# Optimization experiments

Hardware: AMD Instinct MI355X
Metric: run time of the kernel (lower is better)

Reference implementation:

```python
import jax, jax.numpy as jnp
import numpy as np

D_MODEL = 1024
NHEAD = 16
D_FF = 4096
LN_EPS = 1e-5


def _layer_norm(x, g, b):
    mu = jnp.mean(x, axis=-1, keepdims=True)
    var = jnp.mean(jnp.square(x - mu), axis=-1, keepdims=True)
    return (x - mu) * jax.lax.rsqrt(var + LN_EPS) * g + b


def setup_inputs() -> dict:
    key = jax.random.key(0)
    ks = jax.random.split(key, 12)
    d, f = D_MODEL, D_FF
    s = 1.0 / np.sqrt(d)
    inp = {
        "src": jax.random.normal(ks[0], (2, 2048, d), dtype=jnp.float32),
        "Wq": jax.random.uniform(ks[1], (d, d), jnp.float32, -s, s),
        "bq": jnp.zeros((d,), jnp.float32),
        "Wk": jax.random.uniform(ks[2], (d, d), jnp.float32, -s, s),
        "bk": jnp.zeros((d,), jnp.float32),
        "Wv": jax.random.uniform(ks[3], (d, d), jnp.float32, -s, s),
        "bv": jnp.zeros((d,), jnp.float32),
        "Wo": jax.random.uniform(ks[4], (d, d), jnp.float32, -s, s),
        "bo": jnp.zeros((d,), jnp.float32),
        "W1": jax.random.uniform(ks[5], (d, f), jnp.float32, -s, s),
        "b1": jnp.zeros((f,), jnp.float32),
        "W2": jax.random.uniform(ks[6], (f, d), jnp.float32, -1.0 / np.sqrt(f), 1.0 / np.sqrt(f)),
        "b2": jnp.zeros((d,), jnp.float32),
        "ln1_g": jnp.ones((d,), jnp.float32),
        "ln1_b": jnp.zeros((d,), jnp.float32),
        "ln2_g": jnp.ones((d,), jnp.float32),
        "ln2_b": jnp.zeros((d,), jnp.float32),
    }
    return inp


def reference(src, Wq, bq, Wk, bk, Wv, bv, Wo, bo, W1, b1, W2, b2,
              ln1_g, ln1_b, ln2_g, ln2_b):
    B, S, D = src.shape
    H = NHEAD
    hd = D // H
    # QKV projections, split into heads: [B, H, S, hd]
    q = (src @ Wq + bq).reshape(B, S, H, hd).transpose(0, 2, 1, 3)
    k = (src @ Wk + bk).reshape(B, S, H, hd).transpose(0, 2, 1, 3)
    v = (src @ Wv + bv).reshape(B, S, H, hd).transpose(0, 2, 1, 3)
    # Explicit full-score attention (no mask branch), as in source.
    scores = jnp.einsum("bhqd,bhkd->bhqk", q, k) / jnp.sqrt(jnp.asarray(hd, src.dtype))
    attn = jax.nn.softmax(scores, axis=-1)
    ctx = jnp.einsum("bhqk,bhkd->bhqd", attn, v)
    ctx = ctx.transpose(0, 2, 1, 3).reshape(B, S, D)
    src2 = ctx @ Wo + bo
    x = _layer_norm(src + src2, ln1_g, ln1_b)
    ff = jax.nn.relu(x @ W1 + b1) @ W2 + b2
    out = _layer_norm(x + ff, ln2_g, ln2_b)
    return out
```

## Files before the change

### kernel.cpp

```cpp
#include <hip/hip_runtime.h>
#include <cstdint>
#include <cstddef>

#define SEQ 2048
#define BATCH 2
#define ROWS (BATCH * SEQ)

typedef __attribute__((ext_vector_type(8))) short short8;
typedef __attribute__((ext_vector_type(4))) float f32x4;
typedef __attribute__((ext_vector_type(16))) float f32x16;
typedef __attribute__((ext_vector_type(8))) _Float16 half8;
typedef __attribute__((ext_vector_type(2))) __fp16 fp16x2;

__device__ __forceinline__ unsigned short f2bf(float f) {
  union { float f; uint32_t u; } v; v.f = f;
  uint32_t r = v.u + 0x7fffu + ((v.u >> 16) & 1u);
  return (unsigned short)(r >> 16);
}

__device__ __forceinline__ unsigned short bf2h(unsigned short b) {
  union { uint32_t u; float f; } v; v.u = ((uint32_t)b) << 16;
  union { _Float16 h; unsigned short u; } o; o.h = (_Float16)v.f;
  return o.u;
}

__device__ __forceinline__ void async16(const void* g, void* l) {
  __builtin_amdgcn_global_load_lds((const __attribute__((address_space(1))) void*)g,
                                   (__attribute__((address_space(3))) void*)l, 16, 0, 0);
}

__global__ __launch_bounds__(256) void f2bf_kernel(const float* __restrict__ in,
                                                   unsigned short* __restrict__ out) {
  size_t i = ((size_t)blockIdx.x * 256 + threadIdx.x) * 4;
  float4 vv = *(const float4*)(in + i);
  ushort4 o;
  o.x = f2bf(vv.x); o.y = f2bf(vv.y); o.z = f2bf(vv.z); o.w = f2bf(vv.w);
  *(ushort4*)(out + i) = o;
}

__global__ __launch_bounds__(256) void wtrans(const float* __restrict__ W,
                                              unsigned short* __restrict__ WT,
                                              int K, int N, float scale) {
  __shared__ float t[32][33];
  int n0 = blockIdx.x * 32, k0 = blockIdx.y * 32;
  for (int i = threadIdx.y; i < 32; i += 8)
    t[i][threadIdx.x] = W[(size_t)(k0 + i) * N + n0 + threadIdx.x];
  __syncthreads();
  for (int i = threadIdx.y; i < 32; i += 8)
    WT[(size_t)(n0 + i) * K + k0 + threadIdx.x] = f2bf(t[threadIdx.x][i] * scale);
}

__global__ __launch_bounds__(256) void bias_concat(const float* __restrict__ bq,
                                                   const float* __restrict__ bk,
                                                   const float* __restrict__ bv,
                                                   float* __restrict__ o) {
  int i = blockIdx.x * 256 + threadIdx.x;
  float v = (i < 1024) ? bq[i] * 0.18033688f : (i < 2048 ? bk[i - 1024] : bv[i - 2048]);
  o[i] = v;
}

__global__ __launch_bounds__(256) void vtrans(const unsigned short* __restrict__ qkv,
                                              unsigned short* __restrict__ VT) {
  const int st = blockIdx.x, bh = blockIdx.y, b = bh >> 4, h = bh & 15;
  __shared__ unsigned short t[64][72];
  const int tid = threadIdx.x;
#pragma unroll
  for (int it = 0; it < 2; ++it) {
    int i = it * 256 + tid;
    int s = i >> 3, c = (i & 7) * 8;
    short8 v = *(const short8*)(qkv + ((size_t)b * SEQ + st * 64 + s) * 3072 + 2048 + h * 64 + c);
#pragma unroll
    for (int j = 0; j < 8; ++j) t[c + j][s] = bf2h((unsigned short)v[j]);
  }
  __syncthreads();
#pragma unroll
  for (int it = 0; it < 2; ++it) {
    int i = it * 256 + tid;
    int d = i >> 3, sc = (i & 7) * 8;
    short8 o;
#pragma unroll
    for (int j = 0; j < 8; ++j) o[j] = (short)t[d][sc + j];
    *(short8*)(VT + ((size_t)bh * 64 + d) * 2048 + st * 64 + sc) = o;
  }
}

template <bool RELU, bool OUTBF, bool HASRES>
__global__ __launch_bounds__(256) void gemm_bt(
    const unsigned short* __restrict__ A, const unsigned short* __restrict__ BT,
    const float* __restrict__ bias, const float* __restrict__ Rres,
    float* __restrict__ outF, unsigned short* __restrict__ outB,
    int M, int N, int K) {
  __shared__ unsigned short As[2][128 * 32];
  __shared__ unsigned short Bs[2][128 * 32];
  const int tid = threadIdx.x;
  const int lane = tid & 63, ln = lane & 15, quad = lane >> 4;
  const int w = tid >> 6;
  const int m0 = blockIdx.y * 128, n0 = blockIdx.x * 128;
  const int mw = (w >> 1) * 64, nw = (w & 1) * 64;
  f32x4 acc[4][4] = {};
  const int i0 = tid, i1 = tid + 256;
  const int r0 = i0 >> 2, kc0 = (i0 & 3) * 8;
  const int r1 = i1 >> 2, kc1 = (i1 & 3) * 8;
  for (int k0 = 0; k0 < K; k0 += 64) {
    __syncthreads();
#pragma unroll
    for (int p = 0; p < 2; ++p) {
      const int kp = k0 + p * 32;
      async16(A + (size_t)(m0 + r0) * K + kp + kc0, &As[p][i0 * 8]);
      async16(A + (size_t)(m0 + r1) * K + kp + kc1, &As[p][i1 * 8]);
      async16(BT + (size_t)(n0 + r0) * K + kp + kc0, &Bs[p][i0 * 8]);
      async16(BT + (size_t)(n0 + r1) * K + kp + kc1, &Bs[p][i1 * 8]);
    }
    __syncthreads();
#pragma unroll
    for (int p = 0; p < 2; ++p) {
      short8 a[4], b[4];
#pragma unroll
      for (int mi = 0; mi < 4; ++mi)
        a[mi] = *(const short8*)&As[p][(mw + mi * 16 + ln) * 32 + quad * 8];
#pragma unroll
      for (int ni = 0; ni < 4; ++ni)
        b[ni] = *(const short8*)&Bs[p][(nw + ni * 16 + ln) * 32 + quad * 8];
#pragma unroll
      for (int mi = 0; mi < 4; ++mi)
#pragma unroll
        for (int ni = 0; ni < 4; ++ni)
          acc[mi][ni] = __builtin_amdgcn_mfma_f32_16x16x32_bf16(a[mi], b[ni], acc[mi][ni], 0, 0, 0);
    }
  }
#pragma unroll
  for (int mi = 0; mi < 4; ++mi) {
#pragma unroll
    for (int ni = 0; ni < 4; ++ni) {
#pragma unroll
      for (int reg = 0; reg < 4; ++reg) {
        int row = m0 + mw + mi * 16 + quad * 4 + reg;
        int col = n0 + nw + ni * 16 + ln;
        float v = acc[mi][ni][reg] + bias[col];
        if (HASRES) v += Rres[(size_t)row * N + col];
        if (RELU) v = fmaxf(v, 0.f);
        if (OUTBF) outB[(size_t)row * N + col] = f2bf(v);
        else outF[(size_t)row * N + col] = v;
      }
    }
  }
}

template <bool RELU, bool OUTBF, bool HASRES>
__global__ __launch_bounds__(256) void gemm_bt64(
    const unsigned short* __restrict__ A, const unsigned short* __restrict__ BT,
    const float* __restrict__ bias, const float* __restrict__ Rres,
    float* __restrict__ outF, unsigned short* __restrict__ outB,
    int M, int N, int K) {
  __shared__ unsigned short As[4][128 * 32];
  __shared__ unsigned short Bs[4][64 * 32];
  const int tid = threadIdx.x;
  const int lane = tid & 63, ln = lane & 15, quad = lane >> 4;
  const int w = tid >> 6;
  const int m0 = blockIdx.y * 128, n0 = blockIdx.x * 64;
  const int mw = w * 32;
  f32x4 acc[2][4] = {};
  const int i0 = tid, i1 = tid + 256;
  const int r0 = i0 >> 2, kc0 = (i0 & 3) * 8;
  const int r1 = i1 >> 2, kc1 = (i1 & 3) * 8;
  for (int k0 = 0; k0 < K; k0 += 128) {
    __syncthreads();
#pragma unroll
    for (int p = 0; p < 4; ++p) {
      const int kp = k0 + p * 32;
      async16(A + (size_t)(m0 + r0) * K + kp + kc0, &As[p][i0 * 8]);
      async16(A + (size_t)(m0 + r1) * K + kp + kc1, &As[p][i1 * 8]);
      async16(BT + (size_t)(n0 + r0) * K + kp + kc0, &Bs[p][i0 * 8]);
    }
    __syncthreads();
#pragma unroll
    for (int p = 0; p < 4; ++p) {
      short8 a[2], b[4];
#pragma unroll
      for (int mi = 0; mi < 2; ++mi)
        a[mi] = *(const short8*)&As[p][(mw + mi * 16 + ln) * 32 + quad * 8];
#pragma unroll
      for (int ni = 0; ni < 4; ++ni)
        b[ni] = *(const short8*)&Bs[p][(ni * 16 + ln) * 32 + quad * 8];
#pragma unroll
      for (int mi = 0; mi < 2; ++mi)
#pragma unroll
        for (int ni = 0; ni < 4; ++ni)
          acc[mi][ni] = __builtin_amdgcn_mfma_f32_16x16x32_bf16(a[mi], b[ni], acc[mi][ni], 0, 0, 0);
    }
  }
#pragma unroll
  for (int mi = 0; mi < 2; ++mi) {
#pragma unroll
    for (int ni = 0; ni < 4; ++ni) {
#pragma unroll
      for (int reg = 0; reg < 4; ++reg) {
        int row = m0 + mw + mi * 16 + quad * 4 + reg;
        int col = n0 + ni * 16 + ln;
        float v = acc[mi][ni][reg] + bias[col];
        if (HASRES) v += Rres[(size_t)row * N + col];
        if (RELU) v = fmaxf(v, 0.f);
        if (OUTBF) outB[(size_t)row * N + col] = f2bf(v);
        else outF[(size_t)row * N + col] = v;
      }
    }
  }
}

__global__ __launch_bounds__(128, 2) void attn_kernel(const unsigned short* __restrict__ qkv,
                                                      const unsigned short* __restrict__ VT,
                                                      unsigned short* __restrict__ ctx) {
  const int qt = blockIdx.x;
  const int bh = blockIdx.y, b = bh >> 4, h = bh & 15;
  const int tid = threadIdx.x;
  const int w = tid >> 6, lane = tid & 63;
  const int r32 = lane & 31, hi = lane >> 5, r7 = r32 & 7;
  __shared__ __align__(16) unsigned short Ks[2 * 4096];
  __shared__ __align__(16) unsigned short Vs[2 * 4096];
  const size_t rowbase = (size_t)b * SEQ;
  const unsigned short* kbase = qkv + rowbase * 3072 + 1024 + h * 64;
  const unsigned short* vbase = VT + (size_t)bh * 64 * 2048;
  int r_[4], s_[4], wsw_[4];
#pragma unroll
  for (int i = 0; i < 4; ++i) {
    int idx = i * 128 + tid;
    r_[i] = idx >> 3; s_[i] = idx & 7;
    wsw_[i] = r_[i] * 64 + ((s_[i] ^ (r_[i] & 7)) * 8);
  }
  short8 qf[4];
  {
    const unsigned short* qp = qkv + (rowbase + qt * 64 + w * 32 + r32) * 3072 + h * 64;
#pragma unroll
    for (int dc = 0; dc < 4; ++dc) qf[dc] = *(const short8*)(qp + dc * 16 + hi * 8);
  }
  short8 kst[4], vst[4];
#pragma unroll
  for (int i = 0; i < 4; ++i) {
    kst[i] = *(const short8*)(kbase + (size_t)r_[i] * 3072 + s_[i] * 8);
    vst[i] = *(const short8*)(vbase + (size_t)r_[i] * 2048 + s_[i] * 8);
  }
#pragma unroll
  for (int i = 0; i < 4; ++i) {
    *(short8*)&Ks[wsw_[i]] = kst[i];
    *(short8*)&Vs[wsw_[i]] = vst[i];
  }
  __syncthreads();
  f32x16 oacc0 = {}, oacc1 = {};
  float lsum = 0.f;
  int cur = 0;
  for (int kt = 0; kt < 32; ++kt) {
    if (kt < 31) {
      const unsigned short* kp = kbase + (size_t)(kt + 1) * 64 * 3072;
      const unsigned short* vp = vbase + (kt + 1) * 64;
#pragma unroll
      for (int i = 0; i < 4; ++i) {
        kst[i] = *(const short8*)(kp + (size_t)r_[i] * 3072 + s_[i] * 8);
        vst[i] = *(const short8*)(vp + (size_t)r_[i] * 2048 + s_[i] * 8);
      }
    }
    const unsigned short* Kb = &Ks[cur];
    const unsigned short* Vb = &Vs[cur];
    f32x16 z0 = {}, z1 = {};
    __builtin_amdgcn_s_setprio(1);
#pragma unroll
    for (int dc = 0; dc < 4; ++dc) {
      const int sl = ((dc * 2 + hi) ^ r7) * 8;
      short8 kf0 = *(const short8*)&Kb[r32 * 64 + sl];
      short8 kf1 = *(const short8*)&Kb[(32 + r32) * 64 + sl];
      z0 = __builtin_amdgcn_mfma_f32_32x32x16_bf16(kf0, qf[dc], z0, 0, 0, 0);
      z1 = __builtin_amdgcn_mfma_f32_32x32x16_bf16(kf1, qf[dc], z1, 0, 0, 0);
    }
    __builtin_amdgcn_s_setprio(0);
    half8 pf[4];
#pragma unroll
    for (int kc = 0; kc < 4; ++kc) {
      float e[8];
#pragma unroll
      for (int j = 0; j < 8; ++j) {
        float zz = (kc < 2) ? z0[(kc & 1) * 8 + j] : z1[(kc & 1) * 8 + j];
        e[j] = __builtin_amdgcn_exp2f(zz);
        lsum += e[j];
      }
      union { fp16x2 hh; unsigned int u; } a0, a1, b0, b1;
      a0.hh = __builtin_amdgcn_cvt_pkrtz(e[0], e[1]);
      a1.hh = __builtin_amdgcn_cvt_pkrtz(e[2], e[3]);
      b0.hh = __builtin_amdgcn_cvt_pkrtz(e[4], e[5]);
      b1.hh = __builtin_amdgcn_cvt_pkrtz(e[6], e[7]);
      asm volatile("v_permlane32_swap_b32 %0, %1" : "+v"(a0.u), "+v"(b0.u));
      asm volatile("v_permlane32_swap_b32 %0, %1" : "+v"(a1.u), "+v"(b1.u));
      union { unsigned int u[4]; half8 hh; } fr;
      fr.u[0] = a0.u; fr.u[1] = a1.u; fr.u[2] = b0.u; fr.u[3] = b1.u;
      pf[kc] = fr.hh;
    }
    __builtin_amdgcn_s_setprio(1);
#pragma unroll
    for (int kc = 0; kc < 4; ++kc) {
      const int sl = ((kc * 2 + hi) ^ r7) * 8;
      half8 vf0 = *(const half8*)&Vb[r32 * 64 + sl];
      half8 vf1 = *(const half8*)&Vb[(32 + r32) * 64 + sl];
      oacc0 = __builtin_amdgcn_mfma_f32_32x32x16_f16(vf0, pf[kc], oacc0, 0, 0, 0);
      oacc1 = __builtin_amdgcn_mfma_f32_32x32x16_f16(vf1, pf[kc], oacc1, 0, 0, 0);
    }
    __builtin_amdgcn_s_setprio(0);
    if (kt < 31) {
      const int nb = cur ^ 4096;
#pragma unroll
      for (int i = 0; i < 4; ++i) {
        *(short8*)&Ks[nb + wsw_[i]] = kst[i];
        *(short8*)&Vs[nb + wsw_[i]] = vst[i];
      }
      __syncthreads();
      cur = nb;
    }
  }
  float tot = lsum + __shfl_xor(lsum, 32);
  float rl = 1.0f / tot;
  const size_t orow = (rowbase + (size_t)qt * 64 + w * 32 + r32) * 1024 + h * 64 + hi * 4;
#pragma unroll
  for (int tq = 0; tq < 4; ++tq) {
    ushort4 o0, o1;
    o0.x = f2bf(oacc0[tq * 4 + 0] * rl); o0.y = f2bf(oacc0[tq * 4 + 1] * rl);
    o0.z = f2bf(oacc0[tq * 4 + 2] * rl); o0.w = f2bf(oacc0[tq * 4 + 3] * rl);
    *(ushort4*)(ctx + orow + tq * 8) = o0;
    o1.x = f2bf(oacc1[tq * 4 + 0] * rl); o1.y = f2bf(oacc1[tq * 4 + 1] * rl);
    o1.z = f2bf(oacc1[tq * 4 + 2] * rl); o1.w = f2bf(oacc1[tq * 4 + 3] * rl);
    *(ushort4*)(ctx + orow + 32 + tq * 8) = o1;
  }
}

__global__ __launch_bounds__(256) void ln_kernel(const float* __restrict__ y,
                                                 const float* __restrict__ g,
                                                 const float* __restrict__ bb,
                                                 float* __restrict__ outF,
                                                 unsigned short* __restrict__ outB) {
  const int row = blockIdx.x;
  const int tid = threadIdx.x;
  const float* yr = y + (size_t)row * 1024;
  float v[4]; float s = 0.f, s2 = 0.f;
#pragma unroll
  for (int j = 0; j < 4; ++j) {
    v[j] = yr[tid + j * 256];
    s += v[j]; s2 += v[j] * v[j];
  }
#pragma unroll
  for (int off = 1; off < 64; off <<= 1) {
    s += __shfl_xor(s, off);
    s2 += __shfl_xor(s2, off);
  }
  __shared__ float ws1[4], ws2[4];
  if ((tid & 63) == 0) { ws1[tid >> 6] = s; ws2[tid >> 6] = s2; }
  __syncthreads();
  s = ws1[0] + ws1[1] + ws1[2] + ws1[3];
  s2 = ws2[0] + ws2[1] + ws2[2] + ws2[3];
  const float mu = s * (1.f / 1024.f);
  const float var = s2 * (1.f / 1024.f) - mu * mu;
  const float rstd = rsqrtf(var + 1e-5f);
#pragma unroll
  for (int j = 0; j < 4; ++j) {
    int c = tid + j * 256;
    float val = (v[j] - mu) * rstd * g[c] + bb[c];
    if (outF) outF[(size_t)row * 1024 + c] = val;
    if (outB) outB[(size_t)row * 1024 + c] = f2bf(val);
  }
}

extern "C" void kernel_launch(void* const* d_in, const int* in_sizes, int n_in,
                              void* d_out, int out_size, void* d_ws, size_t ws_size,
                              hipStream_t stream) {
  const float* src = (const float*)d_in[0];
  const float* Wq = (const float*)d_in[1];
  const float* bq = (const float*)d_in[2];
  const float* Wk = (const float*)d_in[3];
  const float* bk = (const float*)d_in[4];
  const float* Wv = (const float*)d_in[5];
  const float* bv = (const float*)d_in[6];
  const float* Wo = (const float*)d_in[7];
  const float* bo = (const float*)d_in[8];
  const float* W1 = (const float*)d_in[9];
  const float* b1 = (const float*)d_in[10];
  const float* W2 = (const float*)d_in[11];
  const float* b2 = (const float*)d_in[12];
  const float* ln1g = (const float*)d_in[13];
  const float* ln1b = (const float*)d_in[14];
  const float* ln2g = (const float*)d_in[15];
  const float* ln2b = (const float*)d_in[16];
  float* out = (float*)d_out;

  char* ws = (char*)d_ws;
  unsigned short* qkvT = (unsigned short*)(ws + 0);
  unsigned short* WoT  = (unsigned short*)(ws + 6291456);
  unsigned short* W1T  = (unsigned short*)(ws + 8388608);
  unsigned short* W2T  = (unsigned short*)(ws + 16777216);
  float*          biasq = (float*)(ws + 25165824);
  unsigned short* xbf  = (unsigned short*)(ws + 25178112);
  unsigned short* qkv  = (unsigned short*)(ws + 33566720);
  unsigned short* hbuf = qkv;
  unsigned short* ctx  = (unsigned short*)(ws + 58732544);
  float*          ybuf = (float*)(ws + 67121152);
  unsigned short* VT   = (unsigned short*)(ws + 67121152);
  float*          xf   = (float*)(ws + 83898368);

  const float QSCALE = 0.18033688f;

  f2bf_kernel<<<4096, 256, 0, stream>>>(src, xbf);
  wtrans<<<dim3(32, 32), dim3(32, 8), 0, stream>>>(Wq, qkvT, 1024, 1024, QSCALE);
  wtrans<<<dim3(32, 32), dim3(32, 8), 0, stream>>>(Wk, qkvT + 1024 * 1024, 1024, 1024, 1.0f);
  wtrans<<<dim3(32, 32), dim3(32, 8), 0, stream>>>(Wv, qkvT + 2048 * 1024, 1024, 1024, 1.0f);
  wtrans<<<dim3(32, 32), dim3(32, 8), 0, stream>>>(Wo, WoT, 1024, 1024, 1.0f);
  wtrans<<<dim3(128, 32), dim3(32, 8), 0, stream>>>(W1, W1T, 1024, 4096, 1.0f);
  wtrans<<<dim3(32, 128), dim3(32, 8), 0, stream>>>(W2, W2T, 4096, 1024, 1.0f);
  bias_concat<<<12, 256, 0, stream>>>(bq, bk, bv, biasq);

  gemm_bt<false, true, false><<<dim3(24, 32), 256, 0, stream>>>(
      xbf, qkvT, biasq, nullptr, nullptr, qkv, ROWS, 3072, 1024);
  vtrans<<<dim3(32, 32), 256, 0, stream>>>(qkv, VT);
  attn_kernel<<<dim3(32, 32), 128, 0, stream>>>(qkv, VT, ctx);
  gemm_bt64<false, false, true><<<dim3(16, 32), 256, 0, stream>>>(
      ctx, WoT, bo, src, ybuf, nullptr, ROWS, 1024, 1024);
  ln_kernel<<<4096, 256, 0, stream>>>(ybuf, ln1g, ln1b, xf, xbf);
  gemm_bt<true, true, false><<<dim3(32, 32), 256, 0, stream>>>(
      xbf, W1T, b1, nullptr, nullptr, hbuf, ROWS, 4096, 1024);
  gemm_bt64<false, false, true><<<dim3(16, 32), 256, 0, stream>>>(
      hbuf, W2T, b2, xf, ybuf, nullptr, ROWS, 1024, 4096);
  ln_kernel<<<4096, 256, 0, stream>>>(ybuf, ln2g, ln2b, out, nullptr);
}
```

Before: 393.5 us.

## Split-K the W2 GEMM and fuse partial reduction into final layernorm

The FFN down-projection GEMM (K=4096) now uses a split-K kernel with two K halves, which doubles the number of workgroups so more compute units are occupied. Each half writes fp32 partial sums to a separate buffer. The final layernorm kernel sums the two partials with the bias and residual before normalising, so the epilogue is folded into that kernel. The cost is an extra 16 MB of fp32 partial writes and reads, and the second partial buffer reuses workspace at offset 0, which must not alias live data.

New measurement: 394.6 us. No clear change (+0.3%).

```diff
diff --git a/kernel.cpp b/kernel.cpp
--- a/kernel.cpp
+++ b/kernel.cpp
@@ -205,6 +205,61 @@
       }
     }
   }
+}
+
+__global__ __launch_bounds__(256, 4) void gemm_sk(
+    const unsigned short* __restrict__ A, const unsigned short* __restrict__ BT,
+    float* __restrict__ P0, float* __restrict__ P1,
+    int M, int N, int K, int KH) {
+  __shared__ unsigned short As[2][128 * 32];
+  __shared__ unsigned short Bs[2][64 * 32];
+  const int tid = threadIdx.x;
+  const int lane = tid & 63, ln = lane & 15, quad = lane >> 4;
+  const int w = tid >> 6;
+  const int m0 = blockIdx.y * 128, n0 = blockIdx.x * 64;
+  const int kbeg = blockIdx.z * KH, kend = kbeg + KH;
+  const int mw = w * 32;
+  f32x4 acc[2][4] = {};
+  const int i0 = tid, i1 = tid + 256;
+  const int r0 = i0 >> 2, kc0 = (i0 & 3) * 8;
+  const int r1 = i1 >> 2, kc1 = (i1 & 3) * 8;
+  for (int k0 = kbeg; k0 < kend; k0 += 64) {
+    __syncthreads();
+#pragma unroll
+    for (int p = 0; p < 2; ++p) {
+      const int kp = k0 + p * 32;
+      async16(A + (size_t)(m0 + r0) * K + kp + kc0, &As[p][i0 * 8]);
+      async16(A + (size_t)(m0 + r1) * K + kp + kc1, &As[p][i1 * 8]);
+      async16(BT + (size_t)(n0 + r0) * K + kp + kc0, &Bs[p][i0 * 8]);
+    }
+    __syncthreads();
+#pragma unroll
+    for (int p = 0; p < 2; ++p) {
+      short8 a[2], b[4];
+#pragma unroll
+      for (int mi = 0; mi < 2; ++mi)
+        a[mi] = *(const short8*)&As[p][(mw + mi * 16 + ln) * 32 + quad * 8];
+#pragma unroll
+      for (int ni = 0; ni < 4; ++ni)
+        b[ni] = *(const short8*)&Bs[p][(ni * 16 + ln) * 32 + quad * 8];
+#pragma unroll
+      for (int mi = 0; mi < 2; ++mi)
+#pragma unroll
+        for (int ni = 0; ni < 4; ++ni)
+          acc[mi][ni] = __builtin_amdgcn_mfma_f32_16x16x32_bf16(a[mi], b[ni], acc[mi][ni], 0, 0, 0);
+    }
+  }
+  float* P = blockIdx.z ? P1 : P0;
+#pragma unroll
+  for (int mi = 0; mi < 2; ++mi)
+#pragma unroll
+    for (int ni = 0; ni < 4; ++ni)
+#pragma unroll
+      for (int reg = 0; reg < 4; ++reg) {
+        int row = m0 + mw + mi * 16 + quad * 4 + reg;
+        int col = n0 + ni * 16 + ln;
+        P[(size_t)row * N + col] = acc[mi][ni][reg];
+      }
 }
 
 __global__ __launch_bounds__(128, 2) void attn_kernel(const unsigned short* __restrict__ qkv,
@@ -361,6 +416,43 @@
     float val = (v[j] - mu) * rstd * g[c] + bb[c];
     if (outF) outF[(size_t)row * 1024 + c] = val;
     if (outB) outB[(size_t)row * 1024 + c] = f2bf(val);
+  }
+}
+
+__global__ __launch_bounds__(256) void ln_red_kernel(const float* __restrict__ P0,
+                                                     const float* __restrict__ P1,
+                                                     const float* __restrict__ bias,
+                                                     const float* __restrict__ res,
+                                                     const float* __restrict__ g,
+                                                     const float* __restrict__ bb,
+                                                     float* __restrict__ outF) {
+  const int row = blockIdx.x;
+  const int tid = threadIdx.x;
+  const size_t rb = (size_t)row * 1024;
+  float v[4]; float s = 0.f, s2 = 0.f;
+#pragma unroll
+  for (int j = 0; j < 4; ++j) {
+    int c = tid + j * 256;
+    v[j] = P0[rb + c] + P1[rb + c] + bias[c] + res[rb + c];
+    s += v[j]; s2 += v[j] * v[j];
+  }
+#pragma unroll
+  for (int off = 1; off < 64; off <<= 1) {
+    s += __shfl_xor(s, off);
+    s2 += __shfl_xor(s2, off);
+  }
+  __shared__ float ws1[4], ws2[4];
+  if ((tid & 63) == 0) { ws1[tid >> 6] = s; ws2[tid >> 6] = s2; }
+  __syncthreads();
+  s = ws1[0] + ws1[1] + ws1[2] + ws1[3];
+  s2 = ws2[0] + ws2[1] + ws2[2] + ws2[3];
+  const float mu = s * (1.f / 1024.f);
+  const float var = s2 * (1.f / 1024.f) - mu * mu;
+  const float rstd = rsqrtf(var + 1e-5f);
+#pragma unroll
+  for (int j = 0; j < 4; ++j) {
+    int c = tid + j * 256;
+    outF[rb + c] = (v[j] - mu) * rstd * g[c] + bb[c];
   }
 }
 
@@ -399,6 +491,7 @@
   float*          ybuf = (float*)(ws + 67121152);
   unsigned short* VT   = (unsigned short*)(ws + 67121152);
   float*          xf   = (float*)(ws + 83898368);
+  float*          P1   = (float*)(ws + 0);
 
   const float QSCALE = 0.18033688f;
 
@@ -420,7 +513,7 @@
   ln_kernel<<<4096, 256, 0, stream>>>(ybuf, ln1g, ln1b, xf, xbf);
   gemm_bt<true, true, false><<<dim3(32, 32), 256, 0, stream>>>(
       xbf, W1T, b1, nullptr, nullptr, hbuf, ROWS, 4096, 1024);
-  gemm_bt64<false, false, true><<<dim3(16, 32), 256, 0, stream>>>(
-      hbuf, W2T, b2, xf, ybuf, nullptr, ROWS, 1024, 4096);
-  ln_kernel<<<4096, 256, 0, stream>>>(ybuf, ln2g, ln2b, out, nullptr);
-}
+  gemm_sk<<<dim3(16, 32, 2), 256, 0, stream>>>(
+      hbuf, W2T, ybuf, P1, ROWS, 1024, 4096, 2048);
+  ln_red_kernel<<<4096, 256, 0, stream>>>(ybuf, P1, b2, xf, ln2g, ln2b, out);
+}
```

## Replace QKV and FF1 GEMMs with 256x256-tile software-pipelined kernel

Applied to the files above, without the earlier changes.

Adds a 512-thread GEMM kernel with 256x256 output tiles and double-buffered LDS. It prefetches the next K-tile with async loads while MFMAs run on register-prefetched fragments, and raises wave priority around the MFMA bursts. It replaces the 128x128 gemm_bt for the QKV projection and the first FFN layer. The aim is more data reuse per global load and hidden memory latency, at the cost of far fewer blocks (192 and 256) and 128KB of LDS per block, which caps occupancy at one block per CU.

New measurement: 373.8 us. 1.05x faster.

```diff
diff --git a/kernel.cpp b/kernel.cpp
--- a/kernel.cpp
+++ b/kernel.cpp
@@ -84,66 +84,108 @@
   }
 }
 
-template <bool RELU, bool OUTBF, bool HASRES>
-__global__ __launch_bounds__(256) void gemm_bt(
+template <bool RELU>
+__global__ __launch_bounds__(512, 2) void gemm_8p(
     const unsigned short* __restrict__ A, const unsigned short* __restrict__ BT,
-    const float* __restrict__ bias, const float* __restrict__ Rres,
-    float* __restrict__ outF, unsigned short* __restrict__ outB,
+    const float* __restrict__ bias, unsigned short* __restrict__ outB,
     int M, int N, int K) {
-  __shared__ unsigned short As[2][128 * 32];
-  __shared__ unsigned short Bs[2][128 * 32];
+  __shared__ __align__(16) unsigned short lds[65536];
   const int tid = threadIdx.x;
   const int lane = tid & 63, ln = lane & 15, quad = lane >> 4;
-  const int w = tid >> 6;
-  const int m0 = blockIdx.y * 128, n0 = blockIdx.x * 128;
-  const int mw = (w >> 1) * 64, nw = (w & 1) * 64;
-  f32x4 acc[4][4] = {};
-  const int i0 = tid, i1 = tid + 256;
-  const int r0 = i0 >> 2, kc0 = (i0 & 3) * 8;
-  const int r1 = i1 >> 2, kc1 = (i1 & 3) * 8;
-  for (int k0 = 0; k0 < K; k0 += 64) {
-    __syncthreads();
-#pragma unroll
-    for (int p = 0; p < 2; ++p) {
-      const int kp = k0 + p * 32;
-      async16(A + (size_t)(m0 + r0) * K + kp + kc0, &As[p][i0 * 8]);
-      async16(A + (size_t)(m0 + r1) * K + kp + kc1, &As[p][i1 * 8]);
-      async16(BT + (size_t)(n0 + r0) * K + kp + kc0, &Bs[p][i0 * 8]);
-      async16(BT + (size_t)(n0 + r1) * K + kp + kc1, &Bs[p][i1 * 8]);
-    }
-    __syncthreads();
-#pragma unroll
-    for (int p = 0; p < 2; ++p) {
-      short8 a[4], b[4];
-#pragma unroll
-      for (int mi = 0; mi < 4; ++mi)
-        a[mi] = *(const short8*)&As[p][(mw + mi * 16 + ln) * 32 + quad * 8];
-#pragma unroll
-      for (int ni = 0; ni < 4; ++ni)
-        b[ni] = *(const short8*)&Bs[p][(nw + ni * 16 + ln) * 32 + quad * 8];
-#pragma unroll
-      for (int mi = 0; mi < 4; ++mi)
+  const int wid = tid >> 6, wm = wid >> 2, wn = wid & 3;
+  const int m0 = blockIdx.y * 256, n0 = blockIdx.x * 256;
+  const int srow = tid >> 2, scol = (tid & 3) * 8;
+  const unsigned short* Ag0 = A + (size_t)(m0 + srow) * K + scol;
+  const unsigned short* Ag1 = A + (size_t)(m0 + srow + 128) * K + scol;
+  const unsigned short* Bg0 = BT + (size_t)(n0 + srow) * K + scol;
+  const unsigned short* Bg1 = BT + (size_t)(n0 + srow + 128) * K + scol;
+  const int sdst = tid * 8;
+  f32x4 acc[8][4] = {};
+  short8 fa[2][4];
+  short8 fb[2][4];
+  const int NT = K >> 6;
+#pragma unroll
+  for (int kh = 0; kh < 2; ++kh) {
+    async16(Ag0 + kh * 32, &lds[kh * 8192 + sdst]);
+    async16(Ag1 + kh * 32, &lds[kh * 8192 + sdst + 4096]);
+    async16(Bg0 + kh * 32, &lds[16384 + kh * 8192 + sdst]);
+    async16(Bg1 + kh * 32, &lds[16384 + kh * 8192 + sdst + 4096]);
+  }
+  asm volatile("s_waitcnt vmcnt(0)" ::: "memory");
+  __builtin_amdgcn_s_barrier();
+  {
+    const unsigned short* ab = &lds[0];
+#pragma unroll
+    for (int fi = 0; fi < 4; ++fi)
+      fa[1][fi] = *(const short8*)&ab[(wm * 128 + fi * 16 + ln) * 32 + quad * 8];
+#pragma unroll
+    for (int ni = 0; ni < 4; ++ni)
+      fb[0][ni] = *(const short8*)&ab[16384 + (wn * 64 + ni * 16 + ln) * 32 + quad * 8];
+  }
+  for (int t = 0; t < NT; ++t) {
+    const int cb = (t & 1) * 32768, nb = cb ^ 32768;
+    const bool more = (t + 1 < NT);
+    const int knext = (t + 1) * 64;
+#pragma unroll
+    for (int p = 0; p < 4; ++p) {
+      if (p < 3) {
+        const int kk2 = (p + 1) >> 1, mh2 = (p + 1) & 1;
+        const unsigned short* ab = &lds[cb + kk2 * 8192];
+#pragma unroll
+        for (int fi = 0; fi < 4; ++fi)
+          fa[p & 1][fi] =
+              *(const short8*)&ab[(wm * 128 + mh2 * 64 + fi * 16 + ln) * 32 + quad * 8];
+        if (p == 1) {
+#pragma unroll
+          for (int ni = 0; ni < 4; ++ni)
+            fb[1][ni] = *(const short8*)&ab[16384 + (wn * 64 + ni * 16 + ln) * 32 + quad * 8];
+        }
+      } else if (more) {
+        const unsigned short* ab = &lds[nb];
+#pragma unroll
+        for (int fi = 0; fi < 4; ++fi)
+          fa[1][fi] = *(const short8*)&ab[(wm * 128 + fi * 16 + ln) * 32 + quad * 8];
 #pragma unroll
         for (int ni = 0; ni < 4; ++ni)
-          acc[mi][ni] = __builtin_amdgcn_mfma_f32_16x16x32_bf16(a[mi], b[ni], acc[mi][ni], 0, 0, 0);
-    }
-  }
-#pragma unroll
-  for (int mi = 0; mi < 4; ++mi) {
-#pragma unroll
-    for (int ni = 0; ni < 4; ++ni) {
+          fb[0][ni] = *(const short8*)&ab[16384 + (wn * 64 + ni * 16 + ln) * 32 + quad * 8];
+      }
+      if (more && p < 2) {
+        unsigned short* d = &lds[nb + p * 8192];
+        async16(Ag0 + knext + p * 32, d + sdst);
+        async16(Ag1 + knext + p * 32, d + sdst + 4096);
+        async16(Bg0 + knext + p * 32, d + 16384 + sdst);
+        async16(Bg1 + knext + p * 32, d + 16384 + sdst + 4096);
+      }
+      if (p == 0) {
+        if (more) asm volatile("s_waitcnt vmcnt(4)" ::: "memory");
+        else      asm volatile("s_waitcnt vmcnt(0)" ::: "memory");
+      } else if (p == 2 && more) {
+        asm volatile("s_waitcnt vmcnt(4)" ::: "memory");
+      }
+      __builtin_amdgcn_s_barrier();
+      __builtin_amdgcn_s_setprio(1);
+#pragma unroll
+      for (int fi = 0; fi < 4; ++fi)
+#pragma unroll
+        for (int ni = 0; ni < 4; ++ni)
+          acc[(p & 1) * 4 + fi][ni] = __builtin_amdgcn_mfma_f32_16x16x32_bf16(
+              fa[(p + 1) & 1][fi], fb[p >> 1][ni], acc[(p & 1) * 4 + fi][ni], 0, 0, 0);
+      __builtin_amdgcn_s_setprio(0);
+      if (p < 3 || more) __builtin_amdgcn_s_barrier();
+    }
+  }
+#pragma unroll
+  for (int mi = 0; mi < 8; ++mi)
+#pragma unroll
+    for (int ni = 0; ni < 4; ++ni)
 #pragma unroll
       for (int reg = 0; reg < 4; ++reg) {
-        int row = m0 + mw + mi * 16 + quad * 4 + reg;
-        int col = n0 + nw + ni * 16 + ln;
+        int row = m0 + wm * 128 + mi * 16 + quad * 4 + reg;
+        int col = n0 + wn * 64 + ni * 16 + ln;
         float v = acc[mi][ni][reg] + bias[col];
-        if (HASRES) v += Rres[(size_t)row * N + col];
         if (RELU) v = fmaxf(v, 0.f);
-        if (OUTBF) outB[(size_t)row * N + col] = f2bf(v);
-        else outF[(size_t)row * N + col] = v;
-      }
-    }
-  }
+        outB[(size_t)row * N + col] = f2bf(v);
+      }
 }
 
 template <bool RELU, bool OUTBF, bool HASRES>
@@ -411,15 +453,13 @@
   wtrans<<<dim3(32, 128), dim3(32, 8), 0, stream>>>(W2, W2T, 4096, 1024, 1.0f);
   bias_concat<<<12, 256, 0, stream>>>(bq, bk, bv, biasq);
 
-  gemm_bt<false, true, false><<<dim3(24, 32), 256, 0, stream>>>(
-      xbf, qkvT, biasq, nullptr, nullptr, qkv, ROWS, 3072, 1024);
+  gemm_8p<false><<<dim3(12, 16), 512, 0, stream>>>(xbf, qkvT, biasq, qkv, ROWS, 3072, 1024);
   vtrans<<<dim3(32, 32), 256, 0, stream>>>(qkv, VT);
   attn_kernel<<<dim3(32, 32), 128, 0, stream>>>(qkv, VT, ctx);
   gemm_bt64<false, false, true><<<dim3(16, 32), 256, 0, stream>>>(
       ctx, WoT, bo, src, ybuf, nullptr, ROWS, 1024, 1024);
   ln_kernel<<<4096, 256, 0, stream>>>(ybuf, ln1g, ln1b, xf, xbf);
-  gemm_bt<true, true, false><<<dim3(32, 32), 256, 0, stream>>>(
-      xbf, W1T, b1, nullptr, nullptr, hbuf, ROWS, 4096, 1024);
+  gemm_8p<true><<<dim3(16, 16), 512, 0, stream>>>(xbf, W1T, b1, hbuf, ROWS, 4096, 1024);
   gemm_bt64<false, false, true><<<dim3(16, 32), 256, 0, stream>>>(
       hbuf, W2T, b2, xf, ybuf, nullptr, ROWS, 1024, 4096);
   ln_kernel<<<4096, 256, 0, stream>>>(ybuf, ln2g, ln2b, out, nullptr);
```
